# Optimization experiments

Measured on AMD Instinct MI355X. Metric: run time of the kernel, lower is better.

Reference implementation:

```python
import jax, jax.numpy as jnp
import numpy as np

B, T, C = 2, 1024, 1024
NH, HS, BD, HORIZON = 16, 64, 16, 64


def setup_inputs() -> dict:
    key = jax.random.key(0)
    ks = jax.random.split(key, 16)
    s = 0.02
    return {
        "x": jax.random.normal(ks[0], (B, T, C), jnp.float32),
        "W_disp": jax.random.normal(ks[1], (NH * BD, C), jnp.float32) * s,
        "b_disp": jnp.zeros((NH * BD,), jnp.float32),
        "W_val": jax.random.normal(ks[2], (C, C), jnp.float32) * s,
        "b_val": jnp.zeros((C,), jnp.float32),
        "rel_pos_emb": jax.random.normal(ks[3], (HORIZON, BD), jnp.float32) * s,
        "W_fused": jax.random.normal(ks[4], (2 * BD, BD), jnp.float32) * s,
        "b_fused": jnp.zeros((2 * BD,), jnp.float32),
        "W_pos": jax.random.normal(ks[5], (BD, BD), jnp.float32) * s,
        "W_bond": jax.random.normal(ks[6], (BD,), jnp.float32) * s,
        "b_bond": jnp.zeros((), jnp.float32),
        "W_dmg": jax.random.normal(ks[7], (BD,), jnp.float32) * s,
        "b_dmg": jnp.full((), -3.0, jnp.float32),  # nn.init.constant_(damage_out.bias, -3.0)
        "W_cproj": jax.random.normal(ks[8], (C, C), jnp.float32) * s,
        "b_cproj": jnp.zeros((C,), jnp.float32),
    }


def reference(x, W_disp, b_disp, W_val, b_val, rel_pos_emb, W_fused, b_fused,
              W_pos, W_bond, b_bond, W_dmg, b_dmg, W_cproj, b_cproj):
    delta = min(HORIZON, T)
    gelu = lambda z: jax.nn.gelu(z, approximate=False)  # torch F.gelu default (erf)

    # projections + head split: (B,nh,T,bd) / (B,nh,T,hs)
    disp = (x @ W_disp.T + b_disp).reshape(B, T, NH, BD).transpose(0, 2, 1, 3)
    val = (x @ W_val.T + b_val).reshape(B, T, NH, HS).transpose(0, 2, 1, 3)

    pad = delta - 1
    disp_pad = jnp.pad(disp, ((0, 0), (0, 0), (pad, 0), (0, 0)))
    idx = jnp.arange(T)[:, None] + jnp.arange(delta)[None, :]  # (T,delta) into padded axis
    disp_win = disp_pad[:, :, idx]                      # (B,nh,T,delta,bd)
    strain = disp_win - disp[:, :, :, None, :]          # bond strain

    fused = strain @ W_fused.T + b_fused                # (B,nh,T,delta,2bd)
    bond_f, dmg_f = fused[..., :BD], fused[..., BD:]
    pos_feat = rel_pos_emb[:delta] @ W_pos.T            # (delta,bd)

    bond_logits = gelu(bond_f + pos_feat) @ W_bond + b_bond          # (B,nh,T,delta)
    damage = jax.nn.sigmoid(gelu(dmg_f) @ W_dmg + b_dmg)             # (B,nh,T,delta)
    logits = bond_logits - 10.0 * damage

    cmask = (jnp.arange(T)[:, None] - delta + 1 + jnp.arange(delta)[None, :]) >= 0
    logits = jnp.where(cmask[None, None], logits, -jnp.inf)
    weights = jax.nn.softmax(logits, axis=-1)           # (B,nh,T,delta)

    # weighted sum over window without materializing (B,nh,T,delta,hs)
    val_pad = jnp.pad(val, ((0, 0), (0, 0), (pad, 0), (0, 0)))
    def body(acc, j):
        sl = jax.lax.dynamic_slice_in_dim(val_pad, j, T, axis=2)  # (B,nh,T,hs)
        return acc + weights[..., j][..., None] * sl, None
    out0 = jnp.zeros((B, NH, T, HS), jnp.float32)
    out, _ = jax.lax.scan(body, out0, jnp.arange(delta))

    y = out.transpose(0, 2, 1, 3).reshape(B, T, C)
    return y @ W_cproj.T + b_cproj
```

## Files before the change

### kernel.cpp

```cpp
#include <hip/hip_runtime.h>

#define BDIM 16
#define HSZ 64
#define NHEAD 16
#define DELTA 64
#define LOG2E 1.4426950408889634f

typedef __bf16 bf16x8 __attribute__((ext_vector_type(8)));
typedef float f32x4 __attribute__((ext_vector_type(4)));
typedef float f32x2 __attribute__((ext_vector_type(2)));
typedef unsigned short us8 __attribute__((ext_vector_type(8)));
typedef unsigned int u32;

__device__ __forceinline__ unsigned short f2bf(float f) {
    u32 u = __float_as_uint(f);
    return (unsigned short)((u + 0x7fffu + ((u >> 16) & 1u)) >> 16);
}
__device__ __forceinline__ float bf2f(unsigned short s) {
    return __uint_as_float(((u32)s) << 16);
}

__device__ __forceinline__ void gload_lds16(const void* g, void* l) {
    __builtin_amdgcn_global_load_lds(
        (const __attribute__((address_space(1))) void*)g,
        (__attribute__((address_space(3))) void*)l, 16, 0, 0);
}

__global__ __launch_bounds__(256) void cast4_bf16(
    const float* __restrict__ s0, unsigned short* __restrict__ d0,
    const float* __restrict__ s1, unsigned short* __restrict__ d1,
    const float* __restrict__ s2, unsigned short* __restrict__ d2,
    const float* __restrict__ s3, unsigned short* __restrict__ d3,
    const float* __restrict__ bd, const float* __restrict__ bv,
    float* __restrict__ bcat) {
    int blk = blockIdx.x;
    if (blk == 4352) {
        for (int t = threadIdx.x; t < 320; t += 256) {
            if (t < 64) ((float4*)bcat)[t] = ((const float4*)bd)[t];
            else        ((float4*)bcat)[t] = ((const float4*)bv)[t - 64];
        }
        return;
    }
    const float* src; unsigned short* dst; int base;
    if (blk < 2048)      { src = s0; dst = d0; base = blk; }
    else if (blk < 2304) { src = s1; dst = d1; base = blk - 2048; }
    else if (blk < 3328) { src = s2; dst = d2; base = blk - 2304; }
    else                 { src = s3; dst = d3; base = blk - 3328; }
    int i = base * 256 + threadIdx.x;
    float4 f = ((const float4*)src)[i];
    ushort4 o;
    o.x = f2bf(f.x); o.y = f2bf(f.y); o.z = f2bf(f.z); o.w = f2bf(f.w);
    ((ushort4*)dst)[i] = o;
}

__global__ __launch_bounds__(256) void gemm_bf16(const unsigned short* __restrict__ A,
                                                 const unsigned short* __restrict__ Bw,
                                                 const float* __restrict__ bias,
                                                 float* __restrict__ C,
                                                 unsigned short* __restrict__ CbT,
                                                 int N, int K, int nbx, int mode) {
    __shared__ __align__(16) unsigned short lA[2][8 * 512];
    __shared__ __align__(16) unsigned short lB[2][8 * 512];
    int tid = threadIdx.x;
    int w = tid >> 6, lane = tid & 63;
    int id = blockIdx.x;
    int xcd = id & 7, rr = id >> 3;
    int mi = xcd * 4 + (rr & 3);
    int ni = rr >> 2;
    int bm = mi * 64, bn = ni * 64;
    int wr = w & 1, wc = w >> 1;
    int m16 = lane & 15, q = lane >> 4;

    const unsigned short* aPtr[2];
    const unsigned short* bPtr[2];
#pragma unroll
    for (int i = 0; i < 2; ++i) {
        int g = w + 4 * i;
        aPtr[i] = A + (long)(bm + (g & 3) * 16 + m16) * K + (g >> 2) * 32 + q * 8;
        bPtr[i] = Bw + (long)(bn + (g & 3) * 16 + m16) * K + (g >> 2) * 32 + q * 8;
    }

    f32x4 acc[2][2];
#pragma unroll
    for (int i = 0; i < 2; ++i)
#pragma unroll
        for (int j = 0; j < 2; ++j) acc[i][j] = (f32x4){0.f, 0.f, 0.f, 0.f};

    int nk = K >> 6;
#pragma unroll
    for (int i = 0; i < 2; ++i) {
        gload_lds16(aPtr[i], &lA[0][(w + 4 * i) * 512]);
        gload_lds16(bPtr[i], &lB[0][(w + 4 * i) * 512]);
    }

    for (int kt = 0; kt < nk; ++kt) {
        int p = kt & 1;
        __syncthreads();
        if (kt + 1 < nk) {
            int ko = (kt + 1) * 64;
#pragma unroll
            for (int i = 0; i < 2; ++i) {
                gload_lds16(aPtr[i] + ko, &lA[p ^ 1][(w + 4 * i) * 512]);
                gload_lds16(bPtr[i] + ko, &lB[p ^ 1][(w + 4 * i) * 512]);
            }
        }
#pragma unroll
        for (int s = 0; s < 2; ++s) {
            bf16x8 af[2], bg[2];
#pragma unroll
            for (int r = 0; r < 2; ++r) {
                af[r] = *(const bf16x8*)&lA[p][(s * 4 + wr * 2 + r) * 512 + lane * 8];
                bg[r] = *(const bf16x8*)&lB[p][(s * 4 + wc * 2 + r) * 512 + lane * 8];
            }
#pragma unroll
            for (int r = 0; r < 2; ++r)
#pragma unroll
                for (int n = 0; n < 2; ++n)
                    acc[r][n] = __builtin_amdgcn_mfma_f32_16x16x32_bf16(af[r], bg[n], acc[r][n], 0, 0, 0);
        }
    }

    if (mode == 0 || bn < 256) {
        int ldc = (mode == 0) ? N : 256;
#pragma unroll
        for (int n = 0; n < 2; ++n) {
            int col = bn + wc * 32 + n * 16 + m16;
            float bv = bias[col];
#pragma unroll
            for (int r = 0; r < 2; ++r)
#pragma unroll
                for (int e = 0; e < 4; ++e) {
                    int row = bm + wr * 32 + r * 16 + q * 4 + e;
                    C[(long)row * ldc + col] = acc[r][n][e] + bv;
                }
        }
    } else {
        __syncthreads();
        unsigned short* sC = (unsigned short*)&lA[0][0];
#pragma unroll
        for (int n = 0; n < 2; ++n) {
            int col_l = wc * 32 + n * 16 + m16;
            float bv = bias[bn + col_l];
#pragma unroll
            for (int r = 0; r < 2; ++r)
#pragma unroll
                for (int e = 0; e < 4; ++e) {
                    int row_l = wr * 32 + r * 16 + q * 4 + e;
                    sC[row_l * 64 + col_l] = f2bf(acc[r][n][e] + bv);
                }
        }
        __syncthreads();
        long base0 = ((long)(bm >> 10)) * 1048576 + (long)(bn - 256) * 1024 + (bm & 1023);
#pragma unroll
        for (int it = 0; it < 2; ++it) {
            int slot = it * 256 + tid;
            int hs = slot >> 3;
            int tc = (slot & 7) * 8;
            us8 o;
#pragma unroll
            for (int j = 0; j < 8; ++j) o[j] = sC[(tc + j) * 64 + hs];
            *(us8*)&CbT[base0 + (long)hs * 1024 + tc] = o;
        }
    }
}

__device__ __forceinline__ f32x2 gelu2(f32x2 z) {
    f32x2 z2 = z * z;
    f32x2 u = z * (0.7978845608f + 0.0356774081f * z2);
    f32x2 u2 = u * u;
    f32x2 den = 1.f + 0.33333333f * u2;
    f32x2 r;
    r.x = __builtin_amdgcn_rcpf(den.x);
    r.y = __builtin_amdgcn_rcpf(den.y);
    f32x2 th = u * r;
    f32x2 zh = 0.5f * z;
    return zh + zh * th;
}

#define PROJ_LD 36
#define VW_LD 136

__global__ __launch_bounds__(512) void attn_kernel(
    const float* __restrict__ disp,
    const unsigned short* __restrict__ valT,
    const float* __restrict__ rel,
    const float* __restrict__ Wpos,
    const float* __restrict__ Wf,
    const float* __restrict__ bfu,
    const float* __restrict__ Wb,
    const float* __restrict__ bb_p,
    const float* __restrict__ Wd,
    const float* __restrict__ bd_p,
    unsigned short* __restrict__ y,
    int T) {
    __shared__ __align__(16) unsigned short sWd[64 * VW_LD];
    __shared__ __align__(16) float ov[128 * PROJ_LD + 128 * 16 + 512];
    float* sProj = ov;
    float* sDisp = ov + 128 * PROJ_LD;
    float* sWfT  = sDisp + 128 * 16;
    unsigned short* sValT = (unsigned short*)ov;

    int tid = threadIdx.x;
    int ntile = T / 64;
    int t0 = (blockIdx.x % ntile) * 64;
    int bh = blockIdx.x / ntile;
    int b = bh / NHEAD, h = bh % NHEAD;
    int wave = tid >> 6, lane = tid & 63;
    int m16 = lane & 15, q = lane >> 4;

    {
        uint4 z4 = make_uint4(0, 0, 0, 0);
        for (int i = tid; i < 1088; i += 512) ((uint4*)sWd)[i] = z4;
        sWfT[(tid & 15) * 32 + (tid >> 4)] = Wf[tid];
        {
            int r = tid >> 2, qq = tid & 3;
            int ts = t0 + r - 64;
            float4 v = make_float4(0.f, 0.f, 0.f, 0.f);
            if (ts >= 0)
                v = ((const float4*)(disp + ((long)(b * T + ts) * NHEAD + h) * BDIM))[qq];
            *(float4*)&sDisp[r * 16 + qq * 4] = v;
        }
    }
    __syncthreads();
    for (int idx = tid; idx < 128 * 32; idx += 512) {
        int r = idx >> 5, k = idx & 31;
        float a = 0.f;
#pragma unroll
        for (int d = 0; d < 16; ++d) a += sDisp[r * 16 + d] * sWfT[d * 32 + k];
        sProj[r * PROJ_LD + k] = a;
    }

    float relv[16];
#pragma unroll
    for (int e = 0; e < 4; ++e) {
        float4 rr = ((const float4*)rel)[lane * 4 + e];
        relv[e * 4 + 0] = rr.x; relv[e * 4 + 1] = rr.y;
        relv[e * 4 + 2] = rr.z; relv[e * 4 + 3] = rr.w;
    }
    f32x2 pfd[16], wbd[16];
#pragma unroll
    for (int d = 0; d < 16; ++d) {
        float a = 0.f;
#pragma unroll
        for (int e = 0; e < 16; ++e) a += relv[e] * Wpos[d * 16 + e];
        pfd[d].x = a + bfu[d];
        pfd[d].y = bfu[16 + d];
        wbd[d].x = Wb[d];
        wbd[d].y = Wd[d];
    }
    float bbond = *bb_p, bdmg = *bd_p;
    __syncthreads();

    int wbase = wave * 8;
    for (int rr = 0; rr < 8; ++rr) {
        int tl = wbase + rr;
        int rs = tl + 1 + lane;
        int rc = tl + 64;
        bool valid = (t0 + tl + lane - 63) >= 0;
        float cb[16], cd[16], pb[16], pd[16];
        const float* crow = &sProj[rc * PROJ_LD];
        const float* prow = &sProj[rs * PROJ_LD];
#pragma unroll
        for (int qq = 0; qq < 4; ++qq) {
            float4 v1 = *(const float4*)&crow[qq * 4];
            float4 v2 = *(const float4*)&crow[16 + qq * 4];
            float4 v3 = *(const float4*)&prow[qq * 4];
            float4 v4 = *(const float4*)&prow[16 + qq * 4];
            cb[qq*4+0]=v1.x; cb[qq*4+1]=v1.y; cb[qq*4+2]=v1.z; cb[qq*4+3]=v1.w;
            cd[qq*4+0]=v2.x; cd[qq*4+1]=v2.y; cd[qq*4+2]=v2.z; cd[qq*4+3]=v2.w;
            pb[qq*4+0]=v3.x; pb[qq*4+1]=v3.y; pb[qq*4+2]=v3.z; pb[qq*4+3]=v3.w;
            pd[qq*4+0]=v4.x; pd[qq*4+1]=v4.y; pd[qq*4+2]=v4.z; pd[qq*4+3]=v4.w;
        }
        f32x2 acc2 = (f32x2){bbond, bdmg};
#pragma unroll
        for (int k = 0; k < 16; ++k) {
            f32x2 pz, cz;
            pz.x = pb[k]; pz.y = pd[k];
            cz.x = cb[k]; cz.y = cd[k];
            f32x2 z = pz - cz + pfd[k];
            acc2 = acc2 + gelu2(z) * wbd[k];
        }
        float bl = acc2.x, dm = acc2.y;
        float damage = __builtin_amdgcn_rcpf(1.f + __builtin_exp2f(-dm * LOG2E));
        float logit = bl - 10.f * damage;
        float e = valid ? __builtin_exp2f(logit * LOG2E) : 0.f;
        float ssum = e;
#pragma unroll
        for (int off = 32; off >= 1; off >>= 1) ssum += __shfl_xor(ssum, off);
        sWd[tl * VW_LD + rs] = f2bf(e * __builtin_amdgcn_rcpf(ssum));
    }
    __syncthreads();

    {
        int hs = lane;
        long vbase = ((long)(b * NHEAD * HSZ + h * HSZ + hs)) * T + (t0 - 64);
#pragma unroll
        for (int it = 0; it < 2; ++it) {
            int g = wave * 2 + it;
            int ts0 = t0 - 64 + g * 8;
            us8 v = (us8)0;
            if (ts0 >= 0) v = *(const us8*)&valT[vbase + g * 8];
            *(us8*)&sValT[hs * VW_LD + g * 8] = v;
        }
    }
    __syncthreads();

    {
        int mi = wave >> 1;
        int nh = (wave & 1) * 2;
        int kt0 = mi >> 1;
        f32x4 acc[2];
#pragma unroll
        for (int n = 0; n < 2; ++n) acc[n] = (f32x4){0.f, 0.f, 0.f, 0.f};
#pragma unroll
        for (int kk = 0; kk < 3; ++kk) {
            int kt = kt0 + kk;
            bf16x8 a = *(const bf16x8*)&sWd[(mi * 16 + m16) * VW_LD + kt * 32 + q * 8];
#pragma unroll
            for (int n = 0; n < 2; ++n) {
                bf16x8 bv = *(const bf16x8*)&sValT[((nh + n) * 16 + m16) * VW_LD + kt * 32 + q * 8];
                acc[n] = __builtin_amdgcn_mfma_f32_16x16x32_bf16(a, bv, acc[n], 0, 0, 0);
            }
        }
        int trow = t0 + mi * 16 + q * 4;
#pragma unroll
        for (int n = 0; n < 2; ++n) {
            int col = h * HSZ + (nh + n) * 16 + m16;
#pragma unroll
            for (int e = 0; e < 4; ++e)
                y[(long)(b * T + trow + e) * (NHEAD * HSZ) + col] = f2bf(acc[n][e]);
        }
    }
}

extern "C" void kernel_launch(void* const* d_in, const int* in_sizes, int n_in,
                              void* d_out, int out_size, void* d_ws, size_t ws_size,
                              hipStream_t stream) {
    const float* x       = (const float*)d_in[0];
    const float* W_disp  = (const float*)d_in[1];
    const float* b_disp  = (const float*)d_in[2];
    const float* W_val   = (const float*)d_in[3];
    const float* b_val   = (const float*)d_in[4];
    const float* rel     = (const float*)d_in[5];
    const float* W_fused = (const float*)d_in[6];
    const float* b_fused = (const float*)d_in[7];
    const float* W_pos   = (const float*)d_in[8];
    const float* W_bond  = (const float*)d_in[9];
    const float* b_bond  = (const float*)d_in[10];
    const float* W_dmg   = (const float*)d_in[11];
    const float* b_dmg   = (const float*)d_in[12];
    const float* W_cproj = (const float*)d_in[13];
    const float* b_cproj = (const float*)d_in[14];
    float* out = (float*)d_out;
    float* ws  = (float*)d_ws;

    const int B = 2, T = 1024, C = 1024;
    float* disp = ws;
    float* bcat = disp + 524288;
    unsigned short* x_bf  = (unsigned short*)(bcat + 1280);
    unsigned short* valT  = x_bf + 2097152;
    unsigned short* Wcat  = valT + 2097152;
    unsigned short* Wv_bf = Wcat + 262144;
    unsigned short* Wc_bf = Wv_bf + 1048576;
    unsigned short* y_bf  = x_bf;

    cast4_bf16<<<4353, 256, 0, stream>>>(x, x_bf, W_disp, Wcat, W_val, Wv_bf,
                                         W_cproj, Wc_bf, b_disp, b_val, bcat);

    gemm_bf16<<<640, 256, 0, stream>>>(x_bf, Wcat, bcat, disp, valT,
                                       1280, C, 20, 1);
    attn_kernel<<<dim3(B * NHEAD * (T / 64)), 512, 0, stream>>>(
        disp, valT, rel, W_pos, W_fused, b_fused, W_bond, b_bond, W_dmg, b_dmg,
        y_bf, T);
    gemm_bf16<<<512, 256, 0, stream>>>(y_bf, Wc_bf, b_cproj, out, nullptr,
                                       C, C, 16, 0);
}
```

Measured before the change: 165.7 us.

## Fold W_fused into the displacement projection weights ahead of the GEMM

Precomputes W_fused·W_disp per head in the cast kernel, so the first GEMM directly produces the 32-wide fused projections per head instead of 16-wide displacements. The attention kernel then loads the projections straight into shared memory and drops its per-block small matmul, its barrier and the extra LDS buffers. In exchange the GEMM is wider (1536 columns instead of 1280) and writes twice as much fp32 projection data. b_disp is dropped and the bias zeroed, which is exact only because strain subtracts out any bias. The projections now come from a bf16-rounded product weight, which changes precision slightly.

```diff
diff --git a/kernel.cpp b/kernel.cpp
--- a/kernel.cpp
+++ b/kernel.cpp
@@ -27,25 +27,42 @@
 }
 
 __global__ __launch_bounds__(256) void cast4_bf16(
-    const float* __restrict__ s0, unsigned short* __restrict__ d0,
-    const float* __restrict__ s1, unsigned short* __restrict__ d1,
-    const float* __restrict__ s2, unsigned short* __restrict__ d2,
-    const float* __restrict__ s3, unsigned short* __restrict__ d3,
-    const float* __restrict__ bd, const float* __restrict__ bv,
-    float* __restrict__ bcat) {
+    const float* __restrict__ x, unsigned short* __restrict__ x_bf,
+    const float* __restrict__ Wv, unsigned short* __restrict__ Wv_bf,
+    const float* __restrict__ Wc, unsigned short* __restrict__ Wc_bf,
+    const float* __restrict__ Wdisp, const float* __restrict__ Wf,
+    unsigned short* __restrict__ Wproj,
+    const float* __restrict__ bv, float* __restrict__ bcat) {
     int blk = blockIdx.x;
-    if (blk == 4352) {
-        for (int t = threadIdx.x; t < 320; t += 256) {
-            if (t < 64) ((float4*)bcat)[t] = ((const float4*)bd)[t];
-            else        ((float4*)bcat)[t] = ((const float4*)bv)[t - 64];
+    if (blk == 4096) {
+        for (int t = threadIdx.x; t < 384; t += 256) {
+            float4 v = make_float4(0.f, 0.f, 0.f, 0.f);
+            if (t >= 128) v = ((const float4*)bv)[t - 128];
+            ((float4*)bcat)[t] = v;
         }
         return;
     }
+    if (blk > 4096) {
+        int r = blk - 4097;
+        int h = r >> 5, k = r & 31;
+        int c4 = threadIdx.x;
+        f32x4 acc = (f32x4){0.f, 0.f, 0.f, 0.f};
+#pragma unroll
+        for (int d = 0; d < 16; ++d) {
+            float wf = Wf[k * 16 + d];
+            float4 wd = ((const float4*)Wdisp)[(h * 16 + d) * 256 + c4];
+            acc.x += wf * wd.x; acc.y += wf * wd.y;
+            acc.z += wf * wd.z; acc.w += wf * wd.w;
+        }
+        ushort4 o;
+        o.x = f2bf(acc.x); o.y = f2bf(acc.y); o.z = f2bf(acc.z); o.w = f2bf(acc.w);
+        ((ushort4*)Wproj)[r * 256 + c4] = o;
+        return;
+    }
     const float* src; unsigned short* dst; int base;
-    if (blk < 2048)      { src = s0; dst = d0; base = blk; }
-    else if (blk < 2304) { src = s1; dst = d1; base = blk - 2048; }
-    else if (blk < 3328) { src = s2; dst = d2; base = blk - 2304; }
-    else                 { src = s3; dst = d3; base = blk - 3328; }
+    if (blk < 2048)      { src = x;  dst = x_bf;  base = blk; }
+    else if (blk < 3072) { src = Wv; dst = Wv_bf; base = blk - 2048; }
+    else                 { src = Wc; dst = Wc_bf; base = blk - 3072; }
     int i = base * 256 + threadIdx.x;
     float4 f = ((const float4*)src)[i];
     ushort4 o;
@@ -120,8 +137,8 @@
         }
     }
 
-    if (mode == 0 || bn < 256) {
-        int ldc = (mode == 0) ? N : 256;
+    if (mode == 0 || bn < 512) {
+        int ldc = (mode == 0) ? N : 512;
 #pragma unroll
         for (int n = 0; n < 2; ++n) {
             int col = bn + wc * 32 + n * 16 + m16;
@@ -150,7 +167,7 @@
                 }
         }
         __syncthreads();
-        long base0 = ((long)(bm >> 10)) * 1048576 + (long)(bn - 256) * 1024 + (bm & 1023);
+        long base0 = ((long)(bm >> 10)) * 1048576 + (long)(bn - 512) * 1024 + (bm & 1023);
 #pragma unroll
         for (int it = 0; it < 2; ++it) {
             int slot = it * 256 + tid;
@@ -181,11 +198,10 @@
 #define VW_LD 136
 
 __global__ __launch_bounds__(512) void attn_kernel(
-    const float* __restrict__ disp,
+    const float* __restrict__ projG,
     const unsigned short* __restrict__ valT,
     const float* __restrict__ rel,
     const float* __restrict__ Wpos,
-    const float* __restrict__ Wf,
     const float* __restrict__ bfu,
     const float* __restrict__ Wb,
     const float* __restrict__ bb_p,
@@ -194,10 +210,8 @@
     unsigned short* __restrict__ y,
     int T) {
     __shared__ __align__(16) unsigned short sWd[64 * VW_LD];
-    __shared__ __align__(16) float ov[128 * PROJ_LD + 128 * 16 + 512];
+    __shared__ __align__(16) float ov[128 * PROJ_LD];
     float* sProj = ov;
-    float* sDisp = ov + 128 * PROJ_LD;
-    float* sWfT  = sDisp + 128 * 16;
     unsigned short* sValT = (unsigned short*)ov;
 
     int tid = threadIdx.x;
@@ -211,23 +225,16 @@
     {
         uint4 z4 = make_uint4(0, 0, 0, 0);
         for (int i = tid; i < 1088; i += 512) ((uint4*)sWd)[i] = z4;
-        sWfT[(tid & 15) * 32 + (tid >> 4)] = Wf[tid];
-        {
-            int r = tid >> 2, qq = tid & 3;
+#pragma unroll
+        for (int it = 0; it < 2; ++it) {
+            int i = it * 512 + tid;
+            int r = i >> 3, c4 = i & 7;
             int ts = t0 + r - 64;
             float4 v = make_float4(0.f, 0.f, 0.f, 0.f);
             if (ts >= 0)
-                v = ((const float4*)(disp + ((long)(b * T + ts) * NHEAD + h) * BDIM))[qq];
-            *(float4*)&sDisp[r * 16 + qq * 4] = v;
-        }
-    }
-    __syncthreads();
-    for (int idx = tid; idx < 128 * 32; idx += 512) {
-        int r = idx >> 5, k = idx & 31;
-        float a = 0.f;
-#pragma unroll
-        for (int d = 0; d < 16; ++d) a += sDisp[r * 16 + d] * sWfT[d * 32 + k];
-        sProj[r * PROJ_LD + k] = a;
+                v = ((const float4*)projG)[((long)(b * T + ts)) * 128 + h * 8 + c4];
+            *(float4*)&sProj[r * PROJ_LD + c4 * 4] = v;
+        }
     }
 
     float relv[16];
@@ -355,22 +362,22 @@
     float* ws  = (float*)d_ws;
 
     const int B = 2, T = 1024, C = 1024;
-    float* disp = ws;
-    float* bcat = disp + 524288;
-    unsigned short* x_bf  = (unsigned short*)(bcat + 1280);
+    float* proj = ws;
+    float* bcat = proj + 1048576;
+    unsigned short* x_bf  = (unsigned short*)(bcat + 1536);
     unsigned short* valT  = x_bf + 2097152;
     unsigned short* Wcat  = valT + 2097152;
-    unsigned short* Wv_bf = Wcat + 262144;
-    unsigned short* Wc_bf = Wv_bf + 1048576;
+    unsigned short* Wv_bf = Wcat + 524288;
+    unsigned short* Wc_bf = Wcat + 1572864;
     unsigned short* y_bf  = x_bf;
 
-    cast4_bf16<<<4353, 256, 0, stream>>>(x, x_bf, W_disp, Wcat, W_val, Wv_bf,
-                                         W_cproj, Wc_bf, b_disp, b_val, bcat);
-
-    gemm_bf16<<<640, 256, 0, stream>>>(x_bf, Wcat, bcat, disp, valT,
-                                       1280, C, 20, 1);
+    cast4_bf16<<<4609, 256, 0, stream>>>(x, x_bf, W_val, Wv_bf, W_cproj, Wc_bf,
+                                         W_disp, W_fused, Wcat, b_val, bcat);
+
+    gemm_bf16<<<768, 256, 0, stream>>>(x_bf, Wcat, bcat, proj, valT,
+                                       1536, C, 24, 1);
     attn_kernel<<<dim3(B * NHEAD * (T / 64)), 512, 0, stream>>>(
-        disp, valT, rel, W_pos, W_fused, b_fused, W_bond, b_bond, W_dmg, b_dmg,
+        proj, valT, rel, W_pos, b_fused, W_bond, b_bond, W_dmg, b_dmg,
         y_bf, T);
     gemm_bf16<<<512, 256, 0, stream>>>(y_bf, Wc_bf, b_cproj, out, nullptr,
                                        C, C, 16, 0);
```

Result: no change. 168.3 us (+1.5%).
